# Optimization experiments

Hardware: AMD Instinct MI355X
Metric: run time of the kernel (lower is better)

## Reference

```python
import jax, jax.numpy as jnp
import numpy as np

N_EMBD = 1024
N_HEAD = 16
HEAD_DIM = N_EMBD // N_HEAD
EPS = 1e-5


def _layer_norm(x, g, b):
    mu = jnp.mean(x, axis=-1, keepdims=True)
    var = jnp.mean(jnp.square(x - mu), axis=-1, keepdims=True)
    return (x - mu) * jax.lax.rsqrt(var + EPS) * g + b


def _gelu_new(x):
    # GPT-2 tanh-approximate GELU
    c = np.sqrt(2.0 / np.pi).astype(np.float32)
    return 0.5 * x * (1.0 + jnp.tanh(c * (x + 0.044715 * x ** 3)))


def setup_inputs() -> dict:
    key = jax.random.key(0)
    ks = jax.random.split(key, 8)
    B, S, D = 8, 1024, N_EMBD
    s = 0.02
    return {
        "x": jax.random.normal(ks[0], (B, S, D), jnp.float32),
        "ln1_g": jnp.ones((D,), jnp.float32),
        "ln1_b": jnp.zeros((D,), jnp.float32),
        "c_attn_w": jax.random.normal(ks[1], (D, 3 * D), jnp.float32) * s,
        "c_attn_b": jnp.zeros((3 * D,), jnp.float32),
        "c_proj_w": jax.random.normal(ks[2], (D, D), jnp.float32) * s,
        "c_proj_b": jnp.zeros((D,), jnp.float32),
        "ln2_g": jnp.ones((D,), jnp.float32),
        "ln2_b": jnp.zeros((D,), jnp.float32),
        "fc_w": jax.random.normal(ks[3], (D, 4 * D), jnp.float32) * s,
        "fc_b": jnp.zeros((4 * D,), jnp.float32),
        "proj_w": jax.random.normal(ks[4], (4 * D, D), jnp.float32) * s,
        "proj_b": jnp.zeros((D,), jnp.float32),
    }


def reference(x, ln1_g, ln1_b, c_attn_w, c_attn_b, c_proj_w, c_proj_b,
              ln2_g, ln2_b, fc_w, fc_b, proj_w, proj_b):
    B, S, D = x.shape
    H, Hd = N_HEAD, HEAD_DIM

    residual = x
    h = _layer_norm(x, ln1_g, ln1_b)

    qkv = h @ c_attn_w + c_attn_b          # [B,S,3D]
    q, k, v = jnp.split(qkv, 3, axis=-1)
    # split heads -> [B,H,S,Hd]
    q = q.reshape(B, S, H, Hd).transpose(0, 2, 1, 3)
    k = k.reshape(B, S, H, Hd).transpose(0, 2, 1, 3)
    v = v.reshape(B, S, H, Hd).transpose(0, 2, 1, 3)

    scores = jnp.einsum('bhqd,bhkd->bhqk', q, k) / jnp.sqrt(
        jnp.asarray(Hd, x.dtype))
    causal = jnp.tril(jnp.ones((S, S), bool))
    mask_value = jnp.finfo(scores.dtype).min
    scores = jnp.where(causal, scores, mask_value)
    attn = jax.nn.softmax(scores, axis=-1)
    ctx = jnp.einsum('bhqk,bhkd->bhqd', attn, v)   # [B,H,S,Hd]
    ctx = ctx.transpose(0, 2, 1, 3).reshape(B, S, D)
    attn_out = ctx @ c_proj_w + c_proj_b

    h = residual + attn_out
    residual = h
    h2 = _layer_norm(h, ln2_g, ln2_b)
    ff = _gelu_new(h2 @ fc_w + fc_b) @ proj_w + proj_b
    return residual + ff
```

## Files before the change

### kernel.cpp

```cpp
#include <hip/hip_runtime.h>
#include <cstdint>
#include <cmath>


#define Bb 8
#define Ss 1024
#define Dd 1024
#define Hh 16
#define HD 64
#define MTOK 8192

typedef __attribute__((ext_vector_type(4))) float  floatx4;
typedef __attribute__((ext_vector_type(8))) short  short8;
typedef __attribute__((ext_vector_type(4))) short  short4v;

__device__ __forceinline__ float bf2f(unsigned short u) {
    return __uint_as_float(((unsigned int)u) << 16);
}
__device__ __forceinline__ unsigned short f2bf(float f) {
    unsigned int u = __float_as_uint(f);
    u += 0x7FFFu + ((u >> 16) & 1u);
    return (unsigned short)(u >> 16);
}

__device__ __forceinline__ void gl2lds16(const void* g, void* l) {
    __builtin_amdgcn_global_load_lds(
        (__attribute__((address_space(1))) void*)(g),
        (__attribute__((address_space(3))) void*)(l),
        16, 0, 0);
}

__global__ __launch_bounds__(256) void pack_w(
    const float* __restrict__ W, unsigned short* __restrict__ P, int K, int N)
{
    const int KC = K >> 5;
    int tile = blockIdx.x * 4 + (threadIdx.x >> 6);
    int lane = threadIdx.x & 63;
    int nt = tile / KC, kc = tile - nt * KC;
    int l16 = lane & 15, quad = lane >> 4;
    const float* src = W + (size_t)(kc * 32 + quad * 8) * N + nt * 16 + l16;
    short8 o;
#pragma unroll
    for (int j = 0; j < 8; ++j) o[j] = (short)f2bf(src[(size_t)j * N]);
    *(short8*)(P + ((size_t)(nt * KC + kc) * 64 + lane) * 8) = o;
}

__global__ __launch_bounds__(256) void layernorm_bf16(
    const float* __restrict__ X, const float* __restrict__ g,
    const float* __restrict__ b, unsigned short* __restrict__ Y)
{
    int row = blockIdx.x, t = threadIdx.x;
    const float4* xr = (const float4*)(X + (size_t)row * Dd);
    float4 v = xr[t];
    float s  = v.x + v.y + v.z + v.w;
    float s2 = v.x * v.x + v.y * v.y + v.z * v.z + v.w * v.w;
#pragma unroll
    for (int off = 32; off >= 1; off >>= 1) {
        s  += __shfl_down(s, off, 64);
        s2 += __shfl_down(s2, off, 64);
    }
    __shared__ float red[8];
    int wave = t >> 6, lane = t & 63;
    if (lane == 0) { red[wave] = s; red[4 + wave] = s2; }
    __syncthreads();
    float ts  = red[0] + red[1] + red[2] + red[3];
    float ts2 = red[4] + red[5] + red[6] + red[7];
    float mu  = ts * (1.0f / Dd);
    float var = ts2 * (1.0f / Dd) - mu * mu;
    float rstd = rsqrtf(var + 1e-5f);
    float4 gv = ((const float4*)g)[t];
    float4 bv = ((const float4*)b)[t];
    ushort4 o;
    o.x = f2bf((v.x - mu) * rstd * gv.x + bv.x);
    o.y = f2bf((v.y - mu) * rstd * gv.y + bv.y);
    o.z = f2bf((v.z - mu) * rstd * gv.z + bv.z);
    o.w = f2bf((v.w - mu) * rstd * gv.w + bv.w);
    ((ushort4*)(Y + (size_t)row * Dd))[t] = o;
}

template <int MODE>
__global__ __launch_bounds__(256, 2) void gemm_fw(
    const unsigned short* __restrict__ A,
    const unsigned short* __restrict__ BP,
    const float* __restrict__ bias,
    const float* __restrict__ res,
    void* __restrict__ out,
    int M, int N, int K)
{
    __shared__ short As[128 * 64];
    const int tid  = threadIdx.x;
    const int wave = tid >> 6, lane = tid & 63;
    const int quad = lane >> 4, l16 = lane & 15;
    const int wm = (wave >> 1) * 64, wn = (wave & 1) * 64;
    const int sw = l16 & 7;
    const size_t rowA0 = (size_t)blockIdx.x * 128;
    const int KC = K >> 5;
    const unsigned short* bb = BP
        + ((size_t)(blockIdx.y * 8 + (wave & 1) * 4) * KC * 512 + (size_t)lane * 8);

    floatx4 acc[4][4] = {};

    int srow[4], scs[4];
#pragma unroll
    for (int r = 0; r < 4; ++r) {
        int idx = tid + r * 256;
        srow[r] = idx >> 3;
        scs[r]  = ((idx & 7) ^ (srow[r] & 7)) * 8;
    }

    for (int k0 = 0; k0 < K; k0 += 64) {
#pragma unroll
        for (int r = 0; r < 4; ++r) {
            int idx = tid + r * 256;
            gl2lds16(A + (rowA0 + srow[r]) * K + k0 + scs[r], As + idx * 8);
        }
        const int kc0 = k0 >> 5;
        short8 bfr[2][4];
#pragma unroll
        for (int ks = 0; ks < 2; ++ks)
#pragma unroll
            for (int ni = 0; ni < 4; ++ni)
                bfr[ks][ni] = *(const short8*)(bb
                    + ((size_t)(ni * KC + kc0 + ks) * 512));
        __syncthreads();

#pragma unroll
        for (int ks = 0; ks < 2; ++ks) {
            short8 af[4];
#pragma unroll
            for (int mi = 0; mi < 4; ++mi)
                af[mi] = *(const short8*)(As + (wm + mi * 16 + l16) * 64
                                             + (((ks << 2) + quad) ^ sw) * 8);
#pragma unroll
            for (int mi = 0; mi < 4; ++mi)
#pragma unroll
                for (int ni = 0; ni < 4; ++ni)
                    acc[mi][ni] = __builtin_amdgcn_mfma_f32_16x16x32_bf16(
                        af[mi], bfr[ks][ni], acc[mi][ni], 0, 0, 0);
        }
        __syncthreads();
    }

#pragma unroll
    for (int mi = 0; mi < 4; ++mi) {
#pragma unroll
        for (int ni = 0; ni < 4; ++ni) {
            size_t row = rowA0 + wm + mi * 16 + quad * 4;
            size_t col = (size_t)blockIdx.y * 128 + wn + ni * 16 + l16;
            float bc = bias[col];
#pragma unroll
            for (int r = 0; r < 4; ++r) {
                float v = acc[mi][ni][r] + bc;
                if (MODE == 0) {
                    ((unsigned short*)out)[(row + r) * N + col] = f2bf(v);
                } else if (MODE == 1) {
                    ((float*)out)[(row + r) * N + col] = v + res[(row + r) * N + col];
                } else {
                    float u = 0.7978845608028654f * (v + 0.044715f * v * v * v);
                    float e = __builtin_amdgcn_exp2f(-2.8853900817779268f * u);
                    float gl = v * __builtin_amdgcn_rcpf(1.0f + e);
                    ((unsigned short*)out)[(row + r) * N + col] = f2bf(gl);
                }
            }
        }
    }
}

__global__ __launch_bounds__(256, 2) void attn_mfma(
    const unsigned short* __restrict__ qkv,
    unsigned short* __restrict__ ctx)
{
    __shared__ unsigned short Ks[64 * 72];
    __shared__ unsigned short VT[64 * 72];
    __shared__ unsigned short PT[128 * 72];

    const int tid  = threadIdx.x;
    const int wave = tid >> 6, lane = tid & 63;
    const int quad = lane >> 4, l16 = lane & 15;
    const int blk = blockIdx.x;
    const int c4 = blk & 3, h = (blk >> 2) & 15, b = blk >> 6;
    const size_t tokbase = (size_t)b * Ss;

    const int skey = tid & 63;
    const int sseg = tid >> 6;

    for (int ci = 0; ci < 2; ++ci) {
        const int chunk = ci ? (7 - c4) : c4;
        const int q0 = chunk * 128;

        short8 qf[2][2];
#pragma unroll
        for (int nb = 0; nb < 2; ++nb)
#pragma unroll
            for (int ks = 0; ks < 2; ++ks) {
                const short8* qp = (const short8*)(qkv
                    + (tokbase + q0 + wave * 32 + nb * 16 + l16) * 3072
                    + h * HD + ks * 32 + quad * 8);
                short8 v = *qp, o;
#pragma unroll
                for (int j = 0; j < 8; ++j)
                    o[j] = (short)f2bf(bf2f((unsigned short)v[j]) * 0.18033688011112042f);
                qf[nb][ks] = o;
            }

        floatx4 Oacc[4][2] = {};
        float mrow[2] = {-3.0e38f, -3.0e38f};
        float lrow[2] = {0.f, 0.f};

        const int nkt = 2 * (chunk + 1);
        for (int kt = 0; kt < nkt; ++kt) {
            __syncthreads();
            {
                const short8* kp = (const short8*)(qkv
                    + (tokbase + kt * 64 + skey) * 3072 + Dd + h * HD + sseg * 16);
                short8 k0 = kp[0], k1 = kp[1];
                *(short8*)(Ks + skey * 72 + sseg * 16)     = k0;
                *(short8*)(Ks + skey * 72 + sseg * 16 + 8) = k1;
                const short8* vp = (const short8*)(qkv
                    + (tokbase + kt * 64 + skey) * 3072 + 2 * Dd + h * HD + sseg * 16);
                short8 v0 = vp[0], v1 = vp[1];
#pragma unroll
                for (int j = 0; j < 8; ++j) {
                    VT[(sseg * 16 + j) * 72 + skey]     = (unsigned short)v0[j];
                    VT[(sseg * 16 + 8 + j) * 72 + skey] = (unsigned short)v1[j];
                }
            }
            __syncthreads();

            floatx4 sacc[4][2] = {};
#pragma unroll
            for (int ks = 0; ks < 2; ++ks) {
                short8 af[4];
#pragma unroll
                for (int mi = 0; mi < 4; ++mi)
                    af[mi] = *(const short8*)(Ks + (mi * 16 + l16) * 72 + ks * 32 + quad * 8);
#pragma unroll
                for (int mi = 0; mi < 4; ++mi)
#pragma unroll
                    for (int nb = 0; nb < 2; ++nb)
                        sacc[mi][nb] = __builtin_amdgcn_mfma_f32_16x16x32_bf16(
                            af[mi], qf[nb][ks], sacc[mi][nb], 0, 0, 0);
            }

            if (kt >= 2 * chunk) {
                const int dk = (kt - 2 * chunk) * 64;
#pragma unroll
                for (int nb = 0; nb < 2; ++nb) {
                    int qrow = wave * 32 + nb * 16 + l16;
#pragma unroll
                    for (int mi = 0; mi < 4; ++mi)
#pragma unroll
                        for (int r = 0; r < 4; ++r)
                            if (dk + mi * 16 + quad * 4 + r > qrow)
                                sacc[mi][nb][r] = -3.0e38f;
                }
            }

#pragma unroll
            for (int nb = 0; nb < 2; ++nb) {
                float mx = sacc[0][nb][0];
#pragma unroll
                for (int mi = 0; mi < 4; ++mi)
#pragma unroll
                    for (int r = 0; r < 4; ++r) mx = fmaxf(mx, sacc[mi][nb][r]);
                mx = fmaxf(mx, __shfl_xor(mx, 16, 64));
                mx = fmaxf(mx, __shfl_xor(mx, 32, 64));
                float mnew  = fmaxf(mrow[nb], mx);
                float alpha = __builtin_amdgcn_exp2f(mrow[nb] - mnew);
                float ls = 0.f;
#pragma unroll
                for (int mi = 0; mi < 4; ++mi) {
                    short4v pk;
#pragma unroll
                    for (int r = 0; r < 4; ++r) {
                        float p = __builtin_amdgcn_exp2f(sacc[mi][nb][r] - mnew);
                        ls += p;
                        pk[r] = (short)f2bf(p);
                    }
                    *(short4v*)(PT + (wave * 32 + nb * 16 + l16) * 72 + mi * 16 + quad * 4) = pk;
                }
                ls += __shfl_xor(ls, 16, 64);
                ls += __shfl_xor(ls, 32, 64);
                lrow[nb] = lrow[nb] * alpha + ls;
                mrow[nb] = mnew;
#pragma unroll
                for (int mi3 = 0; mi3 < 4; ++mi3) Oacc[mi3][nb] *= alpha;
            }
            asm volatile("s_waitcnt lgkmcnt(0)" ::: "memory");

#pragma unroll
            for (int ks2 = 0; ks2 < 2; ++ks2) {
                short8 av[4], bp[2];
#pragma unroll
                for (int mi3 = 0; mi3 < 4; ++mi3)
                    av[mi3] = *(const short8*)(VT + (mi3 * 16 + l16) * 72 + ks2 * 32 + quad * 8);
#pragma unroll
                for (int nb = 0; nb < 2; ++nb)
                    bp[nb] = *(const short8*)(PT + (wave * 32 + nb * 16 + l16) * 72 + ks2 * 32 + quad * 8);
#pragma unroll
                for (int mi3 = 0; mi3 < 4; ++mi3)
#pragma unroll
                    for (int nb = 0; nb < 2; ++nb)
                        Oacc[mi3][nb] = __builtin_amdgcn_mfma_f32_16x16x32_bf16(
                            av[mi3], bp[nb], Oacc[mi3][nb], 0, 0, 0);
            }
        }

#pragma unroll
        for (int nb = 0; nb < 2; ++nb) {
            float inv = 1.0f / lrow[nb];
#pragma unroll
            for (int mi3 = 0; mi3 < 4; ++mi3) {
                short4v ov;
#pragma unroll
                for (int r = 0; r < 4; ++r)
                    ov[r] = (short)f2bf(Oacc[mi3][nb][r] * inv);
                *(short4v*)(PT + (wave * 32 + nb * 16 + l16) * 72 + mi3 * 16 + quad * 4) = ov;
            }
        }
        asm volatile("s_waitcnt lgkmcnt(0)" ::: "memory");
        {
            int ql = lane >> 1, dbase = (lane & 1) * 32;
            unsigned short* op = ctx + (tokbase + q0 + wave * 32 + ql) * Dd + h * HD + dbase;
            const unsigned short* lp = PT + (wave * 32 + ql) * 72 + dbase;
#pragma unroll
            for (int i = 0; i < 4; ++i)
                ((short8*)op)[i] = *(const short8*)(lp + i * 8);
        }
    }
}

extern "C" void kernel_launch(void* const* d_in, const int* in_sizes, int n_in,
                              void* d_out, int out_size, void* d_ws, size_t ws_size,
                              hipStream_t stream)
{
    const float* x        = (const float*)d_in[0];
    const float* ln1_g    = (const float*)d_in[1];
    const float* ln1_b    = (const float*)d_in[2];
    const float* c_attn_w = (const float*)d_in[3];
    const float* c_attn_b = (const float*)d_in[4];
    const float* c_proj_w = (const float*)d_in[5];
    const float* c_proj_b = (const float*)d_in[6];
    const float* ln2_g    = (const float*)d_in[7];
    const float* ln2_b    = (const float*)d_in[8];
    const float* fc_w     = (const float*)d_in[9];
    const float* fc_b     = (const float*)d_in[10];
    const float* proj_w   = (const float*)d_in[11];
    const float* proj_b   = (const float*)d_in[12];
    float* out = (float*)d_out;

    char* p = (char*)d_ws;
    auto alloc = [&](size_t bytes) {
        void* r = (void*)p;
        p += (bytes + 255) & ~(size_t)255;
        return r;
    };
    unsigned short* WaP  = (unsigned short*)alloc((size_t)3072 * 1024 * 2);
    unsigned short* WpP  = (unsigned short*)alloc((size_t)1024 * 1024 * 2);
    unsigned short* WfP  = (unsigned short*)alloc((size_t)4096 * 1024 * 2);
    unsigned short* Wp2P = (unsigned short*)alloc((size_t)1024 * 4096 * 2);
    unsigned short* h1   = (unsigned short*)alloc((size_t)MTOK * 1024 * 2);
    unsigned short* qkv  = (unsigned short*)alloc((size_t)MTOK * 3072 * 2);
    unsigned short* ctx  = (unsigned short*)alloc((size_t)MTOK * 1024 * 2);
    float*          hmid = (float*)alloc((size_t)MTOK * 1024 * 4);
    unsigned short* h2   = (unsigned short*)alloc((size_t)MTOK * 1024 * 2);
    unsigned short* ff1  = (unsigned short*)alloc((size_t)MTOK * 4096 * 2);

    pack_w<<<(3072 / 16) * (1024 / 32) / 4, 256, 0, stream>>>(c_attn_w, WaP, 1024, 3072);
    pack_w<<<(1024 / 16) * (1024 / 32) / 4, 256, 0, stream>>>(c_proj_w, WpP, 1024, 1024);
    pack_w<<<(4096 / 16) * (1024 / 32) / 4, 256, 0, stream>>>(fc_w, WfP, 1024, 4096);
    pack_w<<<(1024 / 16) * (4096 / 32) / 4, 256, 0, stream>>>(proj_w, Wp2P, 4096, 1024);

    layernorm_bf16<<<MTOK, 256, 0, stream>>>(x, ln1_g, ln1_b, h1);
    gemm_fw<0><<<dim3(64, 24), 256, 0, stream>>>(h1, WaP, c_attn_b, nullptr, qkv, MTOK, 3072, 1024);
    attn_mfma<<<Bb * Hh * 4, 256, 0, stream>>>(qkv, ctx);
    gemm_fw<1><<<dim3(64, 8), 256, 0, stream>>>(ctx, WpP, c_proj_b, x, hmid, MTOK, 1024, 1024);
    layernorm_bf16<<<MTOK, 256, 0, stream>>>(hmid, ln2_g, ln2_b, h2);
    gemm_fw<2><<<dim3(64, 32), 256, 0, stream>>>(h2, WfP, fc_b, nullptr, ff1, MTOK, 4096, 1024);
    gemm_fw<1><<<dim3(64, 8), 256, 0, stream>>>(ff1, Wp2P, proj_b, hmid, out, MTOK, 1024, 4096);
}
```

Baseline: 460.5 us.

## Replace GEMM with 8-wave triple-buffered pipelined kernel using larger tiles

```diff
diff --git a/kernel.cpp b/kernel.cpp
--- a/kernel.cpp
+++ b/kernel.cpp
@@ -28,6 +28,13 @@
         (__attribute__((address_space(1))) void*)(g),
         (__attribute__((address_space(3))) void*)(l),
         16, 0, 0);
+}
+
+template <int N> __device__ __forceinline__ void wait_vmcnt() {
+    if constexpr (N == 6)       asm volatile("s_waitcnt vmcnt(6)"  ::: "memory");
+    else if constexpr (N == 8)  asm volatile("s_waitcnt vmcnt(8)"  ::: "memory");
+    else if constexpr (N == 12) asm volatile("s_waitcnt vmcnt(12)" ::: "memory");
+    else                        asm volatile("s_waitcnt vmcnt(0)"  ::: "memory");
 }
 
 __global__ __launch_bounds__(256) void pack_w(
@@ -78,8 +85,62 @@
     ((ushort4*)(Y + (size_t)row * Dd))[t] = o;
 }
 
-template <int MODE>
-__global__ __launch_bounds__(256, 2) void gemm_fw(
+
+#define LOADB(TT, KS, DST) do {                                               \
+    const int kc_ = (TT) * 2 + (KS);                                          \
+    _Pragma("unroll")                                                         \
+    for (int n_ = 0; n_ < NI; ++n_)                                           \
+        DST[KS][n_] = *(const short8*)(bbn[n_] + (size_t)kc_ * 512);          \
+} while (0)
+
+#define STAGE2(TT, HALF) do {                                                 \
+    const int bufn_ = ((TT) % 3) * 16384;                                     \
+    _Pragma("unroll")                                                         \
+    for (int r_ = (HALF) * 2; r_ < (HALF) * 2 + 2; ++r_) {                    \
+        int idx_ = tid + r_ * 512;                                            \
+        gl2lds16(sAp[r_] + (size_t)(TT) * 64, As + bufn_ + idx_ * 8);         \
+    }                                                                         \
+} while (0)
+
+#define GPHASE(MH, KS, BC, ISSUE, EXTRAWAIT) do {                             \
+    short8 af[4];                                                             \
+    _Pragma("unroll")                                                         \
+    for (int i_ = 0; i_ < 4; ++i_)                                            \
+        af[i_] = *(const short8*)(As + bufc + aBase + (MH) * 4096             \
+                                  + i_ * 1024 + co[KS]);                      \
+    ISSUE;                                                                    \
+    __builtin_amdgcn_s_barrier();                                             \
+    asm volatile("s_waitcnt lgkmcnt(0)" ::: "memory");                        \
+    EXTRAWAIT;                                                                \
+    __builtin_amdgcn_s_setprio(1);                                            \
+    _Pragma("unroll")                                                         \
+    for (int i_ = 0; i_ < 4; ++i_) {                                          \
+        _Pragma("unroll")                                                     \
+        for (int n_ = 0; n_ < NI; ++n_)                                       \
+            acc[(MH) * 4 + i_][n_] = __builtin_amdgcn_mfma_f32_16x16x32_bf16( \
+                af[i_], BC[KS][n_], acc[(MH) * 4 + i_][n_], 0, 0, 0);         \
+    }                                                                         \
+    __builtin_amdgcn_s_setprio(0);                                            \
+} while (0)
+
+#define GITER(T, BC, BNX) do {                                                \
+    const int tc_ = (T);                                                      \
+    const int tn_ = (tc_ + 1 < NT) ? tc_ + 1 : NT - 1;                        \
+    const int t2_ = (tc_ + 2 < NT) ? tc_ + 2 : NT - 1;                        \
+    const int bufc = (tc_ % 3) * 16384;                                       \
+    GPHASE(0, 0, BC, LOADB(tn_, 0, BNX), wait_vmcnt<NI + 4>());               \
+    __builtin_amdgcn_s_barrier();                                             \
+    GPHASE(1, 0, BC, LOADB(tn_, 1, BNX), (void)0);                            \
+    __builtin_amdgcn_s_barrier();                                             \
+    GPHASE(0, 1, BC, STAGE2(t2_, 0), (void)0);                                \
+    __builtin_amdgcn_s_barrier();                                             \
+    GPHASE(1, 1, BC, STAGE2(t2_, 1), (void)0);                                \
+    wait_vmcnt<2 * NI + 4>();                                                 \
+    __builtin_amdgcn_s_barrier();                                             \
+} while (0)
+
+template <int MODE, int NI>
+__global__ __launch_bounds__(512, 2) void gemm8p(
     const unsigned short* __restrict__ A,
     const unsigned short* __restrict__ BP,
     const float* __restrict__ bias,
@@ -87,66 +148,66 @@
     void* __restrict__ out,
     int M, int N, int K)
 {
-    __shared__ short As[128 * 64];
+    constexpr int BN = 64 * NI;
+    __shared__ short As[3 * 256 * 64];
+
     const int tid  = threadIdx.x;
     const int wave = tid >> 6, lane = tid & 63;
     const int quad = lane >> 4, l16 = lane & 15;
-    const int wm = (wave >> 1) * 64, wn = (wave & 1) * 64;
+    const int wrow = wave >> 2, wcol = wave & 3;
     const int sw = l16 & 7;
-    const size_t rowA0 = (size_t)blockIdx.x * 128;
+    const size_t rowA0 = (size_t)blockIdx.x * 256;
     const int KC = K >> 5;
-    const unsigned short* bb = BP
-        + ((size_t)(blockIdx.y * 8 + (wave & 1) * 4) * KC * 512 + (size_t)lane * 8);
-
-    floatx4 acc[4][4] = {};
-
-    int srow[4], scs[4];
+    const int NT = K >> 6;
+
+    const unsigned short* bbn[NI];
+#pragma unroll
+    for (int ni = 0; ni < NI; ++ni)
+        bbn[ni] = BP
+            + (size_t)(blockIdx.y * (BN / 16) + wcol * NI + ni) * KC * 512
+            + (size_t)lane * 8;
+
+    const unsigned short* sAp[4];
 #pragma unroll
     for (int r = 0; r < 4; ++r) {
-        int idx = tid + r * 256;
-        srow[r] = idx >> 3;
-        scs[r]  = ((idx & 7) ^ (srow[r] & 7)) * 8;
-    }
-
-    for (int k0 = 0; k0 < K; k0 += 64) {
-#pragma unroll
-        for (int r = 0; r < 4; ++r) {
-            int idx = tid + r * 256;
-            gl2lds16(A + (rowA0 + srow[r]) * K + k0 + scs[r], As + idx * 8);
-        }
-        const int kc0 = k0 >> 5;
-        short8 bfr[2][4];
-#pragma unroll
-        for (int ks = 0; ks < 2; ++ks)
-#pragma unroll
-            for (int ni = 0; ni < 4; ++ni)
-                bfr[ks][ni] = *(const short8*)(bb
-                    + ((size_t)(ni * KC + kc0 + ks) * 512));
-        __syncthreads();
-
-#pragma unroll
-        for (int ks = 0; ks < 2; ++ks) {
-            short8 af[4];
-#pragma unroll
-            for (int mi = 0; mi < 4; ++mi)
-                af[mi] = *(const short8*)(As + (wm + mi * 16 + l16) * 64
-                                             + (((ks << 2) + quad) ^ sw) * 8);
-#pragma unroll
-            for (int mi = 0; mi < 4; ++mi)
-#pragma unroll
-                for (int ni = 0; ni < 4; ++ni)
-                    acc[mi][ni] = __builtin_amdgcn_mfma_f32_16x16x32_bf16(
-                        af[mi], bfr[ks][ni], acc[mi][ni], 0, 0, 0);
-        }
-        __syncthreads();
-    }
-
-#pragma unroll
-    for (int mi = 0; mi < 4; ++mi) {
-#pragma unroll
-        for (int ni = 0; ni < 4; ++ni) {
-            size_t row = rowA0 + wm + mi * 16 + quad * 4;
-            size_t col = (size_t)blockIdx.y * 128 + wn + ni * 16 + l16;
+        int idx = tid + r * 512;
+        int sr  = idx >> 3;
+        int sc  = ((idx & 7) ^ (sr & 7)) * 8;
+        sAp[r] = A + (rowA0 + sr) * K + sc;
+    }
+
+    const int aBase = (wrow * 128 + l16) * 64;
+    int co[2];
+    co[0] = ((quad) ^ sw) * 8;
+    co[1] = ((4 + quad) ^ sw) * 8;
+
+    floatx4 acc[8][NI] = {};
+    short8 b0[2][NI], b1[2][NI];
+
+    STAGE2(0, 0);
+    STAGE2(0, 1);
+    LOADB(0, 0, b0);
+    LOADB(0, 1, b0);
+    {
+        const int t1_ = (NT > 1) ? 1 : 0;
+        STAGE2(t1_, 0);
+        STAGE2(t1_, 1);
+    }
+    wait_vmcnt<2 * NI + 4>();
+    __builtin_amdgcn_s_barrier();
+
+    for (int t = 0; t < NT; t += 2) {
+        GITER(t,     b0, b1);
+        GITER(t + 1, b1, b0);
+    }
+
+    const size_t colB = (size_t)blockIdx.y * BN + wcol * (16 * NI);
+#pragma unroll
+    for (int mi = 0; mi < 8; ++mi) {
+#pragma unroll
+        for (int ni = 0; ni < NI; ++ni) {
+            size_t row = rowA0 + wrow * 128 + mi * 16 + quad * 4;
+            size_t col = colB + ni * 16 + l16;
             float bc = bias[col];
 #pragma unroll
             for (int r = 0; r < 4; ++r) {
@@ -372,10 +433,10 @@
     pack_w<<<(1024 / 16) * (4096 / 32) / 4, 256, 0, stream>>>(proj_w, Wp2P, 4096, 1024);
 
     layernorm_bf16<<<MTOK, 256, 0, stream>>>(x, ln1_g, ln1_b, h1);
-    gemm_fw<0><<<dim3(64, 24), 256, 0, stream>>>(h1, WaP, c_attn_b, nullptr, qkv, MTOK, 3072, 1024);
+    gemm8p<0, 2><<<dim3(32, 24), 512, 0, stream>>>(h1, WaP, c_attn_b, nullptr, qkv, MTOK, 3072, 1024);
     attn_mfma<<<Bb * Hh * 4, 256, 0, stream>>>(qkv, ctx);
-    gemm_fw<1><<<dim3(64, 8), 256, 0, stream>>>(ctx, WpP, c_proj_b, x, hmid, MTOK, 1024, 1024);
+    gemm8p<1, 2><<<dim3(32, 8), 512, 0, stream>>>(ctx, WpP, c_proj_b, x, hmid, MTOK, 1024, 1024);
     layernorm_bf16<<<MTOK, 256, 0, stream>>>(hmid, ln2_g, ln2_b, h2);
-    gemm_fw<2><<<dim3(64, 32), 256, 0, stream>>>(h2, WfP, fc_b, nullptr, ff1, MTOK, 4096, 1024);
-    gemm_fw<1><<<dim3(64, 8), 256, 0, stream>>>(ff1, Wp2P, proj_b, hmid, out, MTOK, 1024, 4096);
-}
+    gemm8p<2, 4><<<dim3(32, 16), 512, 0, stream>>>(h2, WfP, fc_b, nullptr, ff1, MTOK, 4096, 1024);
+    gemm8p<1, 2><<<dim3(32, 8), 512, 0, stream>>>(ff1, Wp2P, proj_b, hmid, out, MTOK, 1024, 4096);
+}
```

Result: no change. 467.5 us (+1.5%).

## Replace GEMM with double-buffered 256-row 512-thread kernel staging B through LDS

Applied to the files above, without the earlier changes.

```diff
diff --git a/kernel.cpp b/kernel.cpp
--- a/kernel.cpp
+++ b/kernel.cpp
@@ -28,6 +28,13 @@
         (__attribute__((address_space(1))) void*)(g),
         (__attribute__((address_space(3))) void*)(l),
         16, 0, 0);
+}
+
+template <int N> __device__ __forceinline__ void wait_vmcnt() {
+    if constexpr (N == 6)       asm volatile("s_waitcnt vmcnt(6)"  ::: "memory");
+    else if constexpr (N == 8)  asm volatile("s_waitcnt vmcnt(8)"  ::: "memory");
+    else if constexpr (N == 12) asm volatile("s_waitcnt vmcnt(12)" ::: "memory");
+    else                        asm volatile("s_waitcnt vmcnt(0)"  ::: "memory");
 }
 
 __global__ __launch_bounds__(256) void pack_w(
@@ -78,8 +85,22 @@
     ((ushort4*)(Y + (size_t)row * Dd))[t] = o;
 }
 
-template <int MODE>
-__global__ __launch_bounds__(256, 2) void gemm_fw(
+
+#define V2STAGE(TT) do {                                                      \
+    const int ab_ = ((TT) & 1) * 16384;                                       \
+    _Pragma("unroll")                                                         \
+    for (int r_ = 0; r_ < 4; ++r_)                                            \
+        gl2lds16(sAp[r_] + (size_t)(TT) * 64,                                 \
+                 As + ab_ + (tid + r_ * 512) * 8);                            \
+    const int bb_ = ((TT) & 1) * (BN * 64);                                   \
+    _Pragma("unroll")                                                         \
+    for (int r_ = 0; r_ < LB; ++r_)                                           \
+        gl2lds16(sBp[r_] + (size_t)(TT) * 1024,                               \
+                 Bs + bb_ + (wave * LB + r_) * 512 + lane * 8);               \
+} while (0)
+
+template <int MODE, int WM>
+__global__ __launch_bounds__(512, 2) void gemm_v2(
     const unsigned short* __restrict__ A,
     const unsigned short* __restrict__ BP,
     const float* __restrict__ bias,
@@ -87,66 +108,92 @@
     void* __restrict__ out,
     int M, int N, int K)
 {
-    __shared__ short As[128 * 64];
+    constexpr int WN  = 8 / WM;
+    constexpr int NI  = 4;
+    constexpr int BN  = WN * NI * 16;
+    constexpr int MI  = 16 / WM;
+    constexpr int NPH = (MI * NI * 2) / 16;
+    constexpr int LB  = (BN * 64 * 2) / (512 * 16);
+    constexpr int L   = 4 + LB;
+
+    __shared__ short As[2 * 256 * 64];
+    __shared__ short Bs[2 * BN * 64];
+
     const int tid  = threadIdx.x;
     const int wave = tid >> 6, lane = tid & 63;
     const int quad = lane >> 4, l16 = lane & 15;
-    const int wm = (wave >> 1) * 64, wn = (wave & 1) * 64;
-    const int sw = l16 & 7;
-    const size_t rowA0 = (size_t)blockIdx.x * 128;
+    const int wrow = wave / WN, wcol = wave % WN;
+    const int swA = l16 & 7;
+    const size_t rowA0 = (size_t)blockIdx.x * 256;
     const int KC = K >> 5;
-    const unsigned short* bb = BP
-        + ((size_t)(blockIdx.y * 8 + (wave & 1) * 4) * KC * 512 + (size_t)lane * 8);
-
-    floatx4 acc[4][4] = {};
-
-    int srow[4], scs[4];
+    const int NT = K >> 6;
+
+    const unsigned short* sAp[4];
 #pragma unroll
     for (int r = 0; r < 4; ++r) {
-        int idx = tid + r * 256;
-        srow[r] = idx >> 3;
-        scs[r]  = ((idx & 7) ^ (srow[r] & 7)) * 8;
-    }
-
-    for (int k0 = 0; k0 < K; k0 += 64) {
-#pragma unroll
-        for (int r = 0; r < 4; ++r) {
-            int idx = tid + r * 256;
-            gl2lds16(A + (rowA0 + srow[r]) * K + k0 + scs[r], As + idx * 8);
+        int idx = tid + r * 512;
+        int sr  = idx >> 3;
+        int sc  = ((idx & 7) ^ (sr & 7)) * 8;
+        sAp[r] = A + (rowA0 + sr) * K + sc;
+    }
+    const unsigned short* sBp[LB];
+#pragma unroll
+    for (int r = 0; r < LB; ++r) {
+        int c = wave * LB + r;
+        sBp[r] = BP + ((size_t)(blockIdx.y * (BN / 16) + (c >> 1)) * KC + (c & 1)) * 512
+                    + lane * 8;
+    }
+
+    const int aB = (wrow * (MI * 16) + l16) * 64;
+    const int bB = wcol * NI * 1024 + lane * 8;
+
+    floatx4 acc[MI][NI] = {};
+
+    V2STAGE(0);
+
+    for (int t = 0; t < NT; ++t) {
+        const int tn = (t + 1 < NT) ? t + 1 : t;
+        V2STAGE(tn);
+        wait_vmcnt<L>();
+        __builtin_amdgcn_s_barrier();
+        const int abuf = (t & 1) * 16384;
+        const int bbuf = (t & 1) * (BN * 64);
+        short8 bfr[NI];
+#pragma unroll
+        for (int ph = 0; ph < NPH; ++ph) {
+            const int ks = (NPH == 4) ? (ph >> 1) : ph;
+            const int mh = (NPH == 4) ? (ph & 1) : 0;
+            const int coff = ((ks * 4 + quad) ^ swA) * 8;
+            short8 af[4];
+#pragma unroll
+            for (int i = 0; i < 4; ++i)
+                af[i] = *(const short8*)(As + abuf + aB + mh * 4096
+                                         + i * 1024 + coff);
+            if (mh == 0) {
+#pragma unroll
+                for (int n = 0; n < NI; ++n)
+                    bfr[n] = *(const short8*)(Bs + bbuf + bB + (n * 2 + ks) * 512);
+            }
+            __builtin_amdgcn_s_barrier();
+            __builtin_amdgcn_s_setprio(1);
+#pragma unroll
+            for (int i = 0; i < 4; ++i)
+#pragma unroll
+                for (int n = 0; n < NI; ++n)
+                    acc[mh * 4 + i][n] = __builtin_amdgcn_mfma_f32_16x16x32_bf16(
+                        af[i], bfr[n], acc[mh * 4 + i][n], 0, 0, 0);
+            __builtin_amdgcn_s_setprio(0);
+            __builtin_amdgcn_s_barrier();
         }
-        const int kc0 = k0 >> 5;
-        short8 bfr[2][4];
-#pragma unroll
-        for (int ks = 0; ks < 2; ++ks)
-#pragma unroll
-            for (int ni = 0; ni < 4; ++ni)
-                bfr[ks][ni] = *(const short8*)(bb
-                    + ((size_t)(ni * KC + kc0 + ks) * 512));
-        __syncthreads();
-
-#pragma unroll
-        for (int ks = 0; ks < 2; ++ks) {
-            short8 af[4];
-#pragma unroll
-            for (int mi = 0; mi < 4; ++mi)
-                af[mi] = *(const short8*)(As + (wm + mi * 16 + l16) * 64
-                                             + (((ks << 2) + quad) ^ sw) * 8);
-#pragma unroll
-            for (int mi = 0; mi < 4; ++mi)
-#pragma unroll
-                for (int ni = 0; ni < 4; ++ni)
-                    acc[mi][ni] = __builtin_amdgcn_mfma_f32_16x16x32_bf16(
-                        af[mi], bfr[ks][ni], acc[mi][ni], 0, 0, 0);
-        }
-        __syncthreads();
-    }
-
-#pragma unroll
-    for (int mi = 0; mi < 4; ++mi) {
-#pragma unroll
-        for (int ni = 0; ni < 4; ++ni) {
-            size_t row = rowA0 + wm + mi * 16 + quad * 4;
-            size_t col = (size_t)blockIdx.y * 128 + wn + ni * 16 + l16;
+    }
+
+    const size_t colB = (size_t)blockIdx.y * BN + wcol * (NI * 16);
+#pragma unroll
+    for (int mi = 0; mi < MI; ++mi) {
+#pragma unroll
+        for (int ni = 0; ni < NI; ++ni) {
+            size_t row = rowA0 + wrow * (MI * 16) + mi * 16 + quad * 4;
+            size_t col = colB + ni * 16 + l16;
             float bc = bias[col];
 #pragma unroll
             for (int r = 0; r < 4; ++r) {
@@ -372,10 +419,10 @@
     pack_w<<<(1024 / 16) * (4096 / 32) / 4, 256, 0, stream>>>(proj_w, Wp2P, 4096, 1024);
 
     layernorm_bf16<<<MTOK, 256, 0, stream>>>(x, ln1_g, ln1_b, h1);
-    gemm_fw<0><<<dim3(64, 24), 256, 0, stream>>>(h1, WaP, c_attn_b, nullptr, qkv, MTOK, 3072, 1024);
+    gemm_v2<0, 4><<<dim3(32, 24), 512, 0, stream>>>(h1, WaP, c_attn_b, nullptr, qkv, MTOK, 3072, 1024);
     attn_mfma<<<Bb * Hh * 4, 256, 0, stream>>>(qkv, ctx);
-    gemm_fw<1><<<dim3(64, 8), 256, 0, stream>>>(ctx, WpP, c_proj_b, x, hmid, MTOK, 1024, 1024);
+    gemm_v2<1, 4><<<dim3(32, 8), 512, 0, stream>>>(ctx, WpP, c_proj_b, x, hmid, MTOK, 1024, 1024);
     layernorm_bf16<<<MTOK, 256, 0, stream>>>(hmid, ln2_g, ln2_b, h2);
-    gemm_fw<2><<<dim3(64, 32), 256, 0, stream>>>(h2, WfP, fc_b, nullptr, ff1, MTOK, 4096, 1024);
-    gemm_fw<1><<<dim3(64, 8), 256, 0, stream>>>(ff1, Wp2P, proj_b, hmid, out, MTOK, 1024, 4096);
-}
+    gemm_v2<2, 2><<<dim3(32, 16), 512, 0, stream>>>(h2, WfP, fc_b, nullptr, ff1, MTOK, 4096, 1024);
+    gemm_v2<1, 4><<<dim3(32, 8), 512, 0, stream>>>(ff1, Wp2P, proj_b, hmid, out, MTOK, 1024, 4096);
+}
```

Measured after the change: 511.8 us. +11.1%, slower.

## Replace GEMM with 512-thread 4-stage LDS-pipelined kernel and larger tiles

Applied to the files above, without the earlier changes.

```diff
diff --git a/kernel.cpp b/kernel.cpp
--- a/kernel.cpp
+++ b/kernel.cpp
@@ -28,6 +28,13 @@
         (__attribute__((address_space(1))) void*)(g),
         (__attribute__((address_space(3))) void*)(l),
         16, 0, 0);
+}
+
+template <int N> __device__ __forceinline__ void wait_vmcnt() {
+    if constexpr (N == 6)       asm volatile("s_waitcnt vmcnt(6)"  ::: "memory");
+    else if constexpr (N == 8)  asm volatile("s_waitcnt vmcnt(8)"  ::: "memory");
+    else if constexpr (N == 12) asm volatile("s_waitcnt vmcnt(12)" ::: "memory");
+    else                        asm volatile("s_waitcnt vmcnt(0)"  ::: "memory");
 }
 
 __global__ __launch_bounds__(256) void pack_w(
@@ -78,8 +85,8 @@
     ((ushort4*)(Y + (size_t)row * Dd))[t] = o;
 }
 
-template <int MODE>
-__global__ __launch_bounds__(256, 2) void gemm_fw(
+template <int MODE, int BM>
+__global__ __launch_bounds__(512, 1) void gemm4b(
     const unsigned short* __restrict__ A,
     const unsigned short* __restrict__ BP,
     const float* __restrict__ bias,
@@ -87,66 +94,101 @@
     void* __restrict__ out,
     int M, int N, int K)
 {
-    __shared__ short As[128 * 64];
+    constexpr int MI  = BM / 32;
+    constexpr int NPH = MI / 4;
+    constexpr int LA  = BM / 128;
+    constexpr int ASZ = BM * 32;
+    constexpr int WVC = 2 * (LA + 2);
+    __shared__ short LD[4 * ASZ + 4 * 8192];
+
     const int tid  = threadIdx.x;
     const int wave = tid >> 6, lane = tid & 63;
     const int quad = lane >> 4, l16 = lane & 15;
-    const int wm = (wave >> 1) * 64, wn = (wave & 1) * 64;
-    const int sw = l16 & 7;
-    const size_t rowA0 = (size_t)blockIdx.x * 128;
-    const int KC = K >> 5;
-    const unsigned short* bb = BP
-        + ((size_t)(blockIdx.y * 8 + (wave & 1) * 4) * KC * 512 + (size_t)lane * 8);
-
-    floatx4 acc[4][4] = {};
-
-    int srow[4], scs[4];
-#pragma unroll
-    for (int r = 0; r < 4; ++r) {
-        int idx = tid + r * 256;
-        srow[r] = idx >> 3;
-        scs[r]  = ((idx & 7) ^ (srow[r] & 7)) * 8;
-    }
-
-    for (int k0 = 0; k0 < K; k0 += 64) {
-#pragma unroll
-        for (int r = 0; r < 4; ++r) {
-            int idx = tid + r * 256;
-            gl2lds16(A + (rowA0 + srow[r]) * K + k0 + scs[r], As + idx * 8);
+    const int wrow = wave >> 2, wcol = wave & 3;
+    const size_t rowA0 = (size_t)blockIdx.x * BM;
+    const int NT = K >> 5;
+    const int ntbase = blockIdx.y * 16;
+
+    const unsigned short* aSrc[LA];
+#pragma unroll
+    for (int r = 0; r < LA; ++r) {
+        int idx = tid + r * 512;
+        int rr = idx >> 2, cc = idx & 3;
+        aSrc[r] = A + (rowA0 + rr) * (size_t)K + ((cc ^ ((rr >> 1) & 3)) * 8);
+    }
+    const unsigned short* bSrc[2];
+#pragma unroll
+    for (int r = 0; r < 2; ++r) {
+        int idx = tid + r * 512;
+        bSrc[r] = BP + (size_t)(ntbase + (idx >> 6)) * NT * 512 + (idx & 63) * 8;
+    }
+
+    floatx4 acc[MI][4] = {};
+
+#pragma unroll
+    for (int g = 0; g < 3; ++g) {
+#pragma unroll
+        for (int r = 0; r < LA; ++r)
+            gl2lds16(aSrc[r] + g * 32, LD + g * ASZ + (tid + r * 512) * 8);
+#pragma unroll
+        for (int r = 0; r < 2; ++r)
+            gl2lds16(bSrc[r] + (size_t)g * 512,
+                     LD + 4 * ASZ + g * 8192 + (tid + r * 512) * 8);
+    }
+    wait_vmcnt<WVC>();
+    __builtin_amdgcn_s_barrier();
+
+    const int aswz = (l16 >> 1) & 3;
+    for (int t = 0; t < NT; ++t) {
+        const int buf  = t & 3;
+        const int ts   = (t + 3 < NT) ? t + 3 : NT - 1;
+        const int sbuf = ts & 3;
+        const short* Ab = LD + buf * ASZ;
+        const short* Bt = LD + 4 * ASZ + buf * 8192;
+        short8 bfr[4];
+#pragma unroll
+        for (int n = 0; n < 4; ++n)
+            bfr[n] = *(const short8*)(Bt + ((wcol * 4 + n) * 64 + lane) * 8);
+#pragma unroll
+        for (int mq = 0; mq < NPH; ++mq) {
+            short8 af[4];
+#pragma unroll
+            for (int i = 0; i < 4; ++i) {
+                const int R = wrow * (MI * 16) + mq * 64 + i * 16 + l16;
+                af[i] = *(const short8*)(Ab + R * 32 + ((quad ^ aswz) * 8));
+            }
+            if (NPH == 1 || mq == 0) {
+#pragma unroll
+                for (int r = 0; r < LA; ++r)
+                    gl2lds16(aSrc[r] + (size_t)ts * 32,
+                             LD + sbuf * ASZ + (tid + r * 512) * 8);
+            }
+            if (NPH == 1 || mq == 1) {
+#pragma unroll
+                for (int r = 0; r < 2; ++r)
+                    gl2lds16(bSrc[r] + (size_t)ts * 512,
+                             LD + 4 * ASZ + sbuf * 8192 + (tid + r * 512) * 8);
+                wait_vmcnt<WVC>();
+            }
+            __builtin_amdgcn_s_setprio(1);
+#pragma unroll
+            for (int i = 0; i < 4; ++i)
+#pragma unroll
+                for (int n = 0; n < 4; ++n)
+                    acc[mq * 4 + i][n] = __builtin_amdgcn_mfma_f32_16x16x32_bf16(
+                        af[i], bfr[n], acc[mq * 4 + i][n], 0, 0, 0);
+            __builtin_amdgcn_s_setprio(0);
+            asm volatile("s_barrier" ::: "memory");
         }
-        const int kc0 = k0 >> 5;
-        short8 bfr[2][4];
-#pragma unroll
-        for (int ks = 0; ks < 2; ++ks)
-#pragma unroll
-            for (int ni = 0; ni < 4; ++ni)
-                bfr[ks][ni] = *(const short8*)(bb
-                    + ((size_t)(ni * KC + kc0 + ks) * 512));
-        __syncthreads();
-
-#pragma unroll
-        for (int ks = 0; ks < 2; ++ks) {
-            short8 af[4];
-#pragma unroll
-            for (int mi = 0; mi < 4; ++mi)
-                af[mi] = *(const short8*)(As + (wm + mi * 16 + l16) * 64
-                                             + (((ks << 2) + quad) ^ sw) * 8);
-#pragma unroll
-            for (int mi = 0; mi < 4; ++mi)
-#pragma unroll
-                for (int ni = 0; ni < 4; ++ni)
-                    acc[mi][ni] = __builtin_amdgcn_mfma_f32_16x16x32_bf16(
-                        af[mi], bfr[ks][ni], acc[mi][ni], 0, 0, 0);
-        }
-        __syncthreads();
-    }
-
-#pragma unroll
-    for (int mi = 0; mi < 4; ++mi) {
+    }
+
+    const size_t colB = (size_t)blockIdx.y * 256 + wcol * 64;
+#pragma unroll
+    for (int mi = 0; mi < MI; ++mi) {
 #pragma unroll
         for (int ni = 0; ni < 4; ++ni) {
-            size_t row = rowA0 + wm + mi * 16 + quad * 4;
-            size_t col = (size_t)blockIdx.y * 128 + wn + ni * 16 + l16;
+            size_t row = rowA0 + wrow * (MI * 16) + mi * 16 + quad * 4;
+            size_t col = colB + ni * 16 + l16;
             float bc = bias[col];
 #pragma unroll
             for (int r = 0; r < 4; ++r) {
@@ -372,10 +414,10 @@
     pack_w<<<(1024 / 16) * (4096 / 32) / 4, 256, 0, stream>>>(proj_w, Wp2P, 4096, 1024);
 
     layernorm_bf16<<<MTOK, 256, 0, stream>>>(x, ln1_g, ln1_b, h1);
-    gemm_fw<0><<<dim3(64, 24), 256, 0, stream>>>(h1, WaP, c_attn_b, nullptr, qkv, MTOK, 3072, 1024);
+    gemm4b<0, 128><<<dim3(64, 12), 512, 0, stream>>>(h1, WaP, c_attn_b, nullptr, qkv, MTOK, 3072, 1024);
     attn_mfma<<<Bb * Hh * 4, 256, 0, stream>>>(qkv, ctx);
-    gemm_fw<1><<<dim3(64, 8), 256, 0, stream>>>(ctx, WpP, c_proj_b, x, hmid, MTOK, 1024, 1024);
+    gemm4b<1, 128><<<dim3(64, 4), 512, 0, stream>>>(ctx, WpP, c_proj_b, x, hmid, MTOK, 1024, 1024);
     layernorm_bf16<<<MTOK, 256, 0, stream>>>(hmid, ln2_g, ln2_b, h2);
-    gemm_fw<2><<<dim3(64, 32), 256, 0, stream>>>(h2, WfP, fc_b, nullptr, ff1, MTOK, 4096, 1024);
-    gemm_fw<1><<<dim3(64, 8), 256, 0, stream>>>(ff1, Wp2P, proj_b, hmid, out, MTOK, 1024, 4096);
-}
+    gemm4b<2, 256><<<dim3(32, 16), 512, 0, stream>>>(h2, WfP, fc_b, nullptr, ff1, MTOK, 4096, 1024);
+    gemm4b<1, 128><<<dim3(64, 4), 512, 0, stream>>>(ff1, Wp2P, proj_b, hmid, out, MTOK, 1024, 4096);
+}
```

After: 436.2 us. 5.3% less time.
